# Optimization experiments

Hardware: AMD Instinct MI355X
Metric: run time of the kernel (lower is better)

The kernel has to match this reference:

```python
import jax, jax.numpy as jnp
import numpy as np

H = 16      # num_heads
D = 64      # head_dim
BQ = 64     # block_size_q
BKV = 64    # block_size_kv


def setup_inputs() -> dict:
    key = jax.random.key(0)
    ks = jax.random.split(key, 5)
    B, S, dim = 2, 2048, 1024
    x = jax.random.normal(ks[0], (B, S, dim), dtype=jnp.float32)
    Wq = jax.random.normal(ks[1], (dim, H * D), dtype=jnp.float32) * 0.02
    Wk = jax.random.normal(ks[2], (dim, H * D), dtype=jnp.float32) * 0.02
    Wv = jax.random.normal(ks[3], (dim, H * D), dtype=jnp.float32) * 0.02
    Wo = jax.random.normal(ks[4], (H * D, dim), dtype=jnp.float32) * 0.02
    return {"x": x, "Wq": Wq, "Wk": Wk, "Wv": Wv, "Wo": Wo}


def _flash_tiled(q, k, v, scale):
    # q,k,v: (B, H, S, D). Non-causal tiled attention with online softmax,
    # faithfully replicating the source's per-iteration division by l_new.
    B, nh, S, d = q.shape
    nq, nkv = S // BQ, S // BKV
    qb = q.reshape(B, nh, nq, BQ, d)                       # all q blocks at once (outer loop vectorized)
    kb = k.reshape(B, nh, nkv, BKV, d).transpose(2, 0, 1, 3, 4)  # (nkv, B, H, BKV, D)
    vb = v.reshape(B, nh, nkv, BKV, d).transpose(2, 0, 1, 3, 4)

    o0 = jnp.zeros((B, nh, nq, BQ, d), q.dtype)
    m0 = jnp.full((B, nh, nq, BQ), -jnp.inf, q.dtype)
    l0 = jnp.zeros((B, nh, nq, BQ), q.dtype)

    def step(carry, kv):
        o, m, l = carry
        kj, vj = kv
        s = jnp.einsum('bhnqd,bhkd->bhnqk', qb, kj) * scale   # (B,H,nq,BQ,BKV)
        m_new = jnp.maximum(m, s.max(axis=-1))
        p = jnp.exp(s - m_new[..., None])
        alpha = jnp.exp(m - m_new)
        l_new = alpha * l + p.sum(axis=-1)
        # NOTE: division by l_new every iteration, as in the source module.
        o_new = (alpha[..., None] * o + jnp.einsum('bhnqk,bhkd->bhnqd', p, vj)) / l_new[..., None]
        return (o_new, m_new, l_new), None

    (o, _, _), _ = jax.lax.scan(step, (o0, m0, l0), (kb, vb))
    return o.reshape(B, nh, S, d)


def reference(x, Wq, Wk, Wv, Wo):
    B, S, dim = x.shape
    scale = D ** -0.5
    q = (x @ Wq).reshape(B, S, H, D).transpose(0, 2, 1, 3)
    k = (x @ Wk).reshape(B, S, H, D).transpose(0, 2, 1, 3)
    v = (x @ Wv).reshape(B, S, H, D).transpose(0, 2, 1, 3)
    o = _flash_tiled(q, k, v, scale)                       # (B,H,S,D)
    out = o.transpose(0, 2, 1, 3).reshape(B, S, H * D)
    return out @ Wo
```

## Files before the change

### kernel.cpp

```cpp
#include <hip/hip_runtime.h>
#include <hip/hip_bf16.h>
#include <math.h>

#define BB   2
#define SS   2048
#define DIM  1024
#define NH   16
#define HD   64
#define MTOT (BB * SS)

typedef unsigned short ushortT;
typedef __attribute__((ext_vector_type(8))) short short8v;
typedef __attribute__((ext_vector_type(4))) float float4v;
typedef __attribute__((ext_vector_type(16))) float float16v;

union FragU { short8v v; unsigned short us[8]; unsigned int u[4]; };

__device__ inline unsigned short f2bf(float x) {
    unsigned u = __builtin_bit_cast(unsigned, x);
    u += 0x7fffu + ((u >> 16) & 1u);
    return (unsigned short)(u >> 16);
}
__device__ inline float bf2f(unsigned short h) {
    unsigned u = ((unsigned)h) << 16;
    return __builtin_bit_cast(float, u);
}
__device__ inline void split_tr(float x, unsigned short& hi, unsigned short& lo) {
    unsigned u = __builtin_bit_cast(unsigned, x);
    hi = (unsigned short)(u >> 16);
    float hf = __builtin_bit_cast(float, u & 0xffff0000u);
    lo = (unsigned short)(__builtin_bit_cast(unsigned, x - hf) >> 16);
}
__device__ inline void split4(const float4& x, short4& hi, short4& lo) {
    unsigned short h0 = f2bf(x.x), h1 = f2bf(x.y), h2 = f2bf(x.z), h3 = f2bf(x.w);
    hi = make_short4((short)h0, (short)h1, (short)h2, (short)h3);
    lo = make_short4((short)f2bf(x.x - bf2f(h0)), (short)f2bf(x.y - bf2f(h1)),
                     (short)f2bf(x.z - bf2f(h2)), (short)f2bf(x.w - bf2f(h3)));
}
__device__ inline void gld_lds16(const void* g, void* l) {
    __builtin_amdgcn_global_load_lds(
        (const __attribute__((address_space(1))) void*)g,
        (__attribute__((address_space(3))) void*)l, 16, 0, 0);
}
__device__ inline unsigned cvt_pk_bf16(float a, float b) {
    unsigned r;
    asm("v_cvt_pk_bf16_f32 %0, %1, %2" : "=v"(r) : "v"(a), "v"(b));
    return r;
}
__device__ inline void permlane32_swap(unsigned &a, unsigned &b) {
    asm("v_permlane32_swap_b32 %0, %1" : "+v"(a), "+v"(b));
}

__global__ __launch_bounds__(256) void convert_split_kernel(
    const float* __restrict__ in, ushortT* __restrict__ hi, ushortT* __restrict__ lo, int n4)
{
    int t = blockIdx.x * 256 + threadIdx.x;
    if (t < n4) {
        float4 x = ((const float4*)in)[t];
        short4 h, l; split4(x, h, l);
        ((short4*)hi)[t] = h;
        ((short4*)lo)[t] = l;
    }
}

__global__ __launch_bounds__(256) void transpose_split_kernel(
    const float* __restrict__ W0, const float* __restrict__ W1,
    const float* __restrict__ W2, const float* __restrict__ W3,
    ushortT* __restrict__ WtH, ushortT* __restrict__ WtL)
{
    const int z = blockIdx.z;
    const float* __restrict__ W = (z == 0) ? W0 : (z == 1) ? W1 : (z == 2) ? W2 : W3;
    ushortT* H = WtH + (size_t)z * 1024 * 1024;
    ushortT* L = WtL + (size_t)z * 1024 * 1024;

    __shared__ float T[64][65];
    const int k0 = blockIdx.y * 64, n0 = blockIdx.x * 64;
    const int tid = threadIdx.x;
    const int c4 = (tid & 15) * 4;

#pragma unroll
    for (int i = 0; i < 4; i++) {
        int r = (tid >> 4) + 16 * i;
        *(float4*)&T[r][c4] = *(const float4*)(W + (size_t)(k0 + r) * 1024 + n0 + c4);
    }
    __syncthreads();
#pragma unroll
    for (int i = 0; i < 4; i++) {
        int n = (tid >> 4) + 16 * i;
        float4 vv = make_float4(T[c4 + 0][n], T[c4 + 1][n], T[c4 + 2][n], T[c4 + 3][n]);
        short4 h, l; split4(vv, h, l);
        *(short4*)&H[(size_t)(n0 + n) * 1024 + k0 + c4] = h;
        *(short4*)&L[(size_t)(n0 + n) * 1024 + k0 + c4] = l;
    }
}

__global__ __launch_bounds__(256) void kv_convert_kernel(
    const float* __restrict__ kw,
    ushortT* __restrict__ KhG, ushortT* __restrict__ KlG)
{
    const int jb = blockIdx.x, bh = blockIdx.y;
    const int b = bh >> 4, h = bh & 15;

    __shared__ float T[64][68];
    const int tid = threadIdx.x;
    const size_t ibase = (size_t)b * SS * DIM + (size_t)h * HD + (size_t)(jb * 64) * DIM;
    const int c4 = (tid & 15) * 4;
#pragma unroll
    for (int i = 0; i < 4; i++) {
        int r = (tid >> 4) + 16 * i;
        *(float4*)&T[r][c4] = *(const float4*)(kw + ibase + (size_t)r * DIM + c4);
    }
    __syncthreads();

    ushortT* oh = KhG + (size_t)(bh * 32 + jb) * 4096;
    ushortT* ol = KlG + (size_t)(bh * 32 + jb) * 4096;

#pragma unroll
    for (int i = 0; i < 2; i++) {
        const int s = tid + i * 256;
        const int f = s >> 6;
        const int lane = s & 63;
        const int ds = f >> 1, kvt = f & 1;
        const int kv = kvt * 32 + (lane & 31);
        const int d0 = ds * 16 + (lane >> 5) * 8;
        ushortT hv[8], lv[8];
#pragma unroll
        for (int j = 0; j < 8; j++) split_tr(T[kv][d0 + j], hv[j], lv[j]);
        *(short4*)&oh[s * 8]     = *(short4*)&hv[0];
        *(short4*)&oh[s * 8 + 4] = *(short4*)&hv[4];
        *(short4*)&ol[s * 8]     = *(short4*)&lv[0];
        *(short4*)&ol[s * 8 + 4] = *(short4*)&lv[4];
    }
}

__global__ __launch_bounds__(256, 2) void gemm_bt_split_kernel(
    const ushortT* __restrict__ Ah, const ushortT* __restrict__ Al,
    const ushortT* __restrict__ BtH, const ushortT* __restrict__ BtL,
    float* __restrict__ Y0, float* __restrict__ Y1,
    ushortT* __restrict__ VhG, ushortT* __restrict__ VlG)
{
    const int z = blockIdx.z;
    const ushortT* __restrict__ Bh = BtH + (size_t)z * 1024 * 1024;
    const ushortT* __restrict__ Bl = BtL + (size_t)z * 1024 * 1024;

    const int K = 1024, N = 1024;
    const int m0 = blockIdx.y * 128;
    const int n0 = blockIdx.x * 128;

    __shared__ __align__(16) ushortT AhS[128 * 32];
    __shared__ __align__(16) ushortT AlS[128 * 32];
    __shared__ __align__(16) ushortT BhS[128 * 32];
    __shared__ __align__(16) ushortT BlS[128 * 32];

    const int tid  = threadIdx.x;
    const int wave = tid >> 6, lane = tid & 63;
    const int quad = lane >> 4, l15 = lane & 15;
    const int wm = wave >> 1, wn = wave & 1;

    const int s0 = tid, s1 = tid + 256;
    const int ar0 = s0 >> 2, ak0 = (s0 & 3) * 8;
    const int ar1 = s1 >> 2, ak1 = (s1 & 3) * 8;

    float4v acc[4][4];
#pragma unroll
    for (int i = 0; i < 4; i++)
#pragma unroll
        for (int j = 0; j < 4; j++) acc[i][j] = (float4v){0.f, 0.f, 0.f, 0.f};

    for (int k0 = 0; k0 < K; k0 += 32) {
        __syncthreads();
        gld_lds16(Ah + (size_t)(m0 + ar0) * K + k0 + ak0, &AhS[s0 * 8]);
        gld_lds16(Ah + (size_t)(m0 + ar1) * K + k0 + ak1, &AhS[s1 * 8]);
        gld_lds16(Al + (size_t)(m0 + ar0) * K + k0 + ak0, &AlS[s0 * 8]);
        gld_lds16(Al + (size_t)(m0 + ar1) * K + k0 + ak1, &AlS[s1 * 8]);
        gld_lds16(Bh + (size_t)(n0 + ar0) * K + k0 + ak0, &BhS[s0 * 8]);
        gld_lds16(Bh + (size_t)(n0 + ar1) * K + k0 + ak1, &BhS[s1 * 8]);
        gld_lds16(Bl + (size_t)(n0 + ar0) * K + k0 + ak0, &BlS[s0 * 8]);
        gld_lds16(Bl + (size_t)(n0 + ar1) * K + k0 + ak1, &BlS[s1 * 8]);
        __syncthreads();

        FragU ah[4], al[4], bh[4], bl[4];
#pragma unroll
        for (int t = 0; t < 4; t++) {
            ah[t].v = *(const short8v*)&AhS[(wm * 64 + t * 16 + l15) * 32 + quad * 8];
            al[t].v = *(const short8v*)&AlS[(wm * 64 + t * 16 + l15) * 32 + quad * 8];
            bh[t].v = *(const short8v*)&BhS[(wn * 64 + t * 16 + l15) * 32 + quad * 8];
            bl[t].v = *(const short8v*)&BlS[(wn * 64 + t * 16 + l15) * 32 + quad * 8];
        }
#pragma unroll
        for (int mt = 0; mt < 4; mt++)
#pragma unroll
            for (int nt = 0; nt < 4; nt++) {
                acc[mt][nt] = __builtin_amdgcn_mfma_f32_16x16x32_bf16(ah[mt].v, bh[nt].v, acc[mt][nt], 0, 0, 0);
                acc[mt][nt] = __builtin_amdgcn_mfma_f32_16x16x32_bf16(ah[mt].v, bl[nt].v, acc[mt][nt], 0, 0, 0);
                acc[mt][nt] = __builtin_amdgcn_mfma_f32_16x16x32_bf16(al[mt].v, bh[nt].v, acc[mt][nt], 0, 0, 0);
            }
    }

    if (z == 2) {
        const int b  = m0 >> 11;
        const int jb = ((m0 & 2047) >> 6) + wm;
        const int h  = (n0 >> 6) + wn;
        const size_t tb = (size_t)((b * 16 + h) * 32 + jb) * 4096;
        ushortT* vh = VhG + tb;
        ushortT* vl = VlG + tb;
#pragma unroll
        for (int mt = 0; mt < 4; mt++)
#pragma unroll
            for (int nt = 0; nt < 4; nt++) {
                const int off = ((((nt >> 1) * 4 + mt) * 64 +
                                  (quad >> 1) * 32 + (nt & 1) * 16 + l15) * 8) +
                                (quad & 1) * 4;
                float4 vv = make_float4(acc[mt][nt][0], acc[mt][nt][1],
                                        acc[mt][nt][2], acc[mt][nt][3]);
                unsigned short h0, l0, h1, l1, h2, l2, h3, l3;
                split_tr(vv.x, h0, l0); split_tr(vv.y, h1, l1);
                split_tr(vv.z, h2, l2); split_tr(vv.w, h3, l3);
                *(short4*)&vh[off] = make_short4((short)h0, (short)h1, (short)h2, (short)h3);
                *(short4*)&vl[off] = make_short4((short)l0, (short)l1, (short)l2, (short)l3);
            }
    } else {
        float* __restrict__ Y = (z == 0) ? Y0 : Y1;
#pragma unroll
        for (int mt = 0; mt < 4; mt++)
#pragma unroll
            for (int r = 0; r < 4; r++) {
                const int row = m0 + wm * 64 + mt * 16 + quad * 4 + r;
                float* yp = Y + (size_t)row * N + n0 + wn * 64 + l15;
#pragma unroll
                for (int nt = 0; nt < 4; nt++)
                    yp[nt * 16] = acc[mt][nt][r];
            }
    }
}

__global__ __launch_bounds__(256, 2) void attn_mfma_kernel(
    const float* __restrict__ q,
    const ushortT* __restrict__ KhG, const ushortT* __restrict__ KlG,
    const ushortT* __restrict__ VhG, const ushortT* __restrict__ VlG,
    ushortT* __restrict__ Oh, ushortT* __restrict__ Ol)
{
    __shared__ __align__(16) ushortT SMEM[32768];

    const int tid  = threadIdx.x;
    const int wave = tid >> 6, lane = tid & 63;
    const int l31 = lane & 31, hi5 = lane >> 5;
    const int bh = blockIdx.y, b = bh >> 4, h = bh & 15;
    const size_t base = (size_t)b * SS * DIM + (size_t)h * HD;
    const int qs0 = blockIdx.x * 128 + wave * 32;
    const int lane8 = lane * 8;
    const int sl0 = wave * 128 + lane, sl1 = sl0 + 64;

    ushortT* K0 = SMEM;
    ushortT* K1 = SMEM + 8192;
    ushortT* V0 = SMEM + 16384;
    ushortT* V1 = SMEM + 24576;

    const float qscale = 0.125f * 1.4426950408889634f;
    FragU Qh[4], Ql[4];
    {
        const int qrow = qs0 + l31;
#pragma unroll
        for (int ds = 0; ds < 4; ds++) {
            const float* p0 = q + base + (size_t)qrow * DIM + ds * 16 + hi5 * 8;
            float4 a = *(const float4*)(p0);
            float4 c = *(const float4*)(p0 + 4);
            float e[8] = {a.x, a.y, a.z, a.w, c.x, c.y, c.z, c.w};
#pragma unroll
            for (int j = 0; j < 8; j++) {
                float x = e[j] * qscale;
                unsigned short hs = f2bf(x);
                Qh[ds].us[j] = hs;
                Ql[ds].us[j] = f2bf(x - bf2f(hs));
            }
        }
    }

    float16v Oacc[2];
#pragma unroll
    for (int dt = 0; dt < 2; dt++)
        Oacc[dt] = (float16v){0.f,0.f,0.f,0.f,0.f,0.f,0.f,0.f,
                              0.f,0.f,0.f,0.f,0.f,0.f,0.f,0.f};

    float m_run = -INFINITY;
    float l_run = 0.f;

    auto stage_K = [&](int t, ushortT* dst) {
        const size_t tb = (size_t)(bh * 32 + t) * 4096;
        gld_lds16(KhG + tb + sl0 * 8, &dst[sl0 * 8]);
        gld_lds16(KhG + tb + sl1 * 8, &dst[sl1 * 8]);
        gld_lds16(KlG + tb + sl0 * 8, &dst[4096 + sl0 * 8]);
        gld_lds16(KlG + tb + sl1 * 8, &dst[4096 + sl1 * 8]);
    };
    auto stage_V = [&](int t, ushortT* dst) {
        const size_t tb = (size_t)(bh * 32 + t) * 4096;
        gld_lds16(VhG + tb + sl0 * 8, &dst[sl0 * 8]);
        gld_lds16(VhG + tb + sl1 * 8, &dst[sl1 * 8]);
        gld_lds16(VlG + tb + sl0 * 8, &dst[4096 + sl0 * 8]);
        gld_lds16(VlG + tb + sl1 * 8, &dst[4096 + sl1 * 8]);
    };

    auto qk = [&](const ushortT* Kb, float16v (&st)[2]) {
        const ushortT* KhS = Kb;
        const ushortT* KlS = Kb + 4096;
#pragma unroll
        for (int t = 0; t < 2; t++)
            st[t] = (float16v){0.f,0.f,0.f,0.f,0.f,0.f,0.f,0.f,
                               0.f,0.f,0.f,0.f,0.f,0.f,0.f,0.f};
#pragma unroll
        for (int ds = 0; ds < 4; ds++) {
            FragU kh0, kl0, kh1, kl1;
            kh0.v = *(const short8v*)&KhS[(ds * 2 + 0) * 512 + lane8];
            kl0.v = *(const short8v*)&KlS[(ds * 2 + 0) * 512 + lane8];
            kh1.v = *(const short8v*)&KhS[(ds * 2 + 1) * 512 + lane8];
            kl1.v = *(const short8v*)&KlS[(ds * 2 + 1) * 512 + lane8];
            st[0] = __builtin_amdgcn_mfma_f32_32x32x16_bf16(kh0.v, Qh[ds].v, st[0], 0, 0, 0);
            st[0] = __builtin_amdgcn_mfma_f32_32x32x16_bf16(kh0.v, Ql[ds].v, st[0], 0, 0, 0);
            st[0] = __builtin_amdgcn_mfma_f32_32x32x16_bf16(kl0.v, Qh[ds].v, st[0], 0, 0, 0);
            st[1] = __builtin_amdgcn_mfma_f32_32x32x16_bf16(kh1.v, Qh[ds].v, st[1], 0, 0, 0);
            st[1] = __builtin_amdgcn_mfma_f32_32x32x16_bf16(kh1.v, Ql[ds].v, st[1], 0, 0, 0);
            st[1] = __builtin_amdgcn_mfma_f32_32x32x16_bf16(kl1.v, Qh[ds].v, st[1], 0, 0, 0);
        }
    };

    auto finish = [&](float16v (&st)[2], const ushortT* Vb) {
        const ushortT* VhS = Vb;
        const ushortT* VlS = Vb + 4096;
        float oscale, inv;
        {
            float g[8];
#pragma unroll
            for (int t = 0; t < 2; t++)
#pragma unroll
                for (int i = 0; i < 4; i++)
                    g[t * 4 + i] = fmaxf(fmaxf(st[t][4 * i], st[t][4 * i + 1]),
                                         fmaxf(st[t][4 * i + 2], st[t][4 * i + 3]));
            float vmax = fmaxf(fmaxf(fmaxf(g[0], g[1]), fmaxf(g[2], g[3])),
                               fmaxf(fmaxf(g[4], g[5]), fmaxf(g[6], g[7])));
            vmax = fmaxf(vmax, __shfl_xor(vmax, 32, 64));
            const float mn = fmaxf(m_run, vmax);
            const float al = __builtin_amdgcn_exp2f(m_run - mn);

            float ssum = 0.f;
#pragma unroll
            for (int t = 0; t < 2; t++)
#pragma unroll
                for (int r = 0; r < 16; r++) {
                    const float p = __builtin_amdgcn_exp2f(st[t][r] - mn);
                    st[t][r] = p;
                    ssum += p;
                }
            ssum += __shfl_xor(ssum, 32, 64);
            const float ln = al * l_run + ssum;
            inv = __builtin_amdgcn_rcpf(ln);
            oscale = al * inv;
#pragma unroll
            for (int t = 0; t < 2; t++)
#pragma unroll
                for (int r = 0; r < 16; r++)
                    st[t][r] *= inv;
            m_run = mn;
            l_run = ln;
        }

#pragma unroll
        for (int dt = 0; dt < 2; dt++)
#pragma unroll
            for (int r = 0; r < 16; r++)
                Oacc[dt][r] *= oscale;

#pragma unroll
        for (int kvs = 0; kvs < 4; kvs++) {
            const int kvt = kvs >> 1;
            const int R = (kvs & 1) * 8;
            float p0 = st[kvt][R + 0], p1 = st[kvt][R + 1];
            float p2 = st[kvt][R + 2], p3 = st[kvt][R + 3];
            float p4 = st[kvt][R + 4], p5 = st[kvt][R + 5];
            float p6 = st[kvt][R + 6], p7 = st[kvt][R + 7];
            unsigned X0 = cvt_pk_bf16(p0, p1), X1 = cvt_pk_bf16(p2, p3);
            unsigned Y0 = cvt_pk_bf16(p4, p5), Y1 = cvt_pk_bf16(p6, p7);
            float e0 = p0 - __builtin_bit_cast(float, X0 << 16);
            float e1 = p1 - __builtin_bit_cast(float, X0 & 0xffff0000u);
            float e2 = p2 - __builtin_bit_cast(float, X1 << 16);
            float e3 = p3 - __builtin_bit_cast(float, X1 & 0xffff0000u);
            float e4 = p4 - __builtin_bit_cast(float, Y0 << 16);
            float e5 = p5 - __builtin_bit_cast(float, Y0 & 0xffff0000u);
            float e6 = p6 - __builtin_bit_cast(float, Y1 << 16);
            float e7 = p7 - __builtin_bit_cast(float, Y1 & 0xffff0000u);
            unsigned Z0 = cvt_pk_bf16(e0, e1), Z1 = cvt_pk_bf16(e2, e3);
            unsigned W0 = cvt_pk_bf16(e4, e5), W1 = cvt_pk_bf16(e6, e7);
            permlane32_swap(X0, Y0);
            permlane32_swap(X1, Y1);
            permlane32_swap(Z0, W0);
            permlane32_swap(Z1, W1);
            FragU Phf, Plf;
            Phf.u[0] = X0; Phf.u[1] = X1; Phf.u[2] = Y0; Phf.u[3] = Y1;
            Plf.u[0] = Z0; Plf.u[1] = Z1; Plf.u[2] = W0; Plf.u[3] = W1;

#pragma unroll
            for (int dt = 0; dt < 2; dt++) {
                FragU vh, vl;
                vh.v = *(const short8v*)&VhS[(dt * 4 + kvs) * 512 + lane8];
                vl.v = *(const short8v*)&VlS[(dt * 4 + kvs) * 512 + lane8];
                Oacc[dt] = __builtin_amdgcn_mfma_f32_32x32x16_bf16(vh.v, Phf.v, Oacc[dt], 0, 0, 0);
                Oacc[dt] = __builtin_amdgcn_mfma_f32_32x32x16_bf16(vl.v, Phf.v, Oacc[dt], 0, 0, 0);
                Oacc[dt] = __builtin_amdgcn_mfma_f32_32x32x16_bf16(vh.v, Plf.v, Oacc[dt], 0, 0, 0);
            }
        }
    };

    float16v stA[2], stB[2];

    stage_K(0, K0);
    stage_K(1, K1);
    stage_V(0, V0);
    __syncthreads();
    qk(K0, stA);
    __syncthreads();

    auto iter = [&](int jb, float16v (&SC)[2], float16v (&SN)[2],
                    ushortT* Kc, ushortT* Kn, ushortT* Vc, ushortT* Vn) {
        if (jb <= 29) stage_K(jb + 2, Kc);
        if (jb <= 30) stage_V(jb + 1, Vn);
        if (jb <= 30) qk(Kn, SN);
        finish(SC, Vc);
        __syncthreads();
    };

    for (int jb = 0; jb < 32; jb += 2) {
        iter(jb,     stA, stB, K0, K1, V0, V1);
        iter(jb + 1, stB, stA, K1, K0, V1, V0);
    }

    float* EP = ((float*)SMEM) + wave * 1056;
    const int qq = lane >> 1, dh = (lane & 1) * 16;
#pragma unroll
    for (int dt = 0; dt < 2; dt++) {
#pragma unroll
        for (int g = 0; g < 4; g++) {
            float4 wv = make_float4(Oacc[dt][4 * g + 0], Oacc[dt][4 * g + 1],
                                    Oacc[dt][4 * g + 2], Oacc[dt][4 * g + 3]);
            *(float4*)&EP[l31 * 33 + g * 8 + hi5 * 4] = wv;
        }
        float vals[16];
#pragma unroll
        for (int k4 = 0; k4 < 4; k4++)
            *(float4*)&vals[k4 * 4] = *(const float4*)&EP[qq * 33 + dh + k4 * 4];

        unsigned ho[8], lo8[8];
#pragma unroll
        for (int kk = 0; kk < 8; kk++) {
            unsigned short h0, l0, h1, l1;
            split_tr(vals[2 * kk], h0, l0);
            split_tr(vals[2 * kk + 1], h1, l1);
            ho[kk]  = (unsigned)h0 | ((unsigned)h1 << 16);
            lo8[kk] = (unsigned)l0 | ((unsigned)l1 << 16);
        }
        const int qrow = qs0 + qq;
        const size_t off = (size_t)(b * SS + qrow) * DIM + h * HD + dt * 32 + dh;
        *(uint4*)&Oh[off]     = make_uint4(ho[0], ho[1], ho[2], ho[3]);
        *(uint4*)&Oh[off + 8] = make_uint4(ho[4], ho[5], ho[6], ho[7]);
        *(uint4*)&Ol[off]     = make_uint4(lo8[0], lo8[1], lo8[2], lo8[3]);
        *(uint4*)&Ol[off + 8] = make_uint4(lo8[4], lo8[5], lo8[6], lo8[7]);
    }
}

extern "C" void kernel_launch(void* const* d_in, const int* in_sizes, int n_in,
                              void* d_out, int out_size, void* d_ws, size_t ws_size,
                              hipStream_t stream)
{
    const float* x  = (const float*)d_in[0];
    const float* Wq = (const float*)d_in[1];
    const float* Wk = (const float*)d_in[2];
    const float* Wv = (const float*)d_in[3];
    const float* Wo = (const float*)d_in[4];
    float* out = (float*)d_out;

    char* w = (char*)d_ws;
    float*   qw  = (float*)(w);
    float*   kw  = (float*)(w + ((size_t)16 << 20));
    ushortT* VhG = (ushortT*)(w + ((size_t)32 << 20));
    ushortT* VlG = (ushortT*)(w + ((size_t)40 << 20));
    ushortT* XhS = (ushortT*)(w + ((size_t)48 << 20));
    ushortT* XlS = (ushortT*)(w + ((size_t)56 << 20));
    ushortT* WtH = (ushortT*)(w + ((size_t)64 << 20));
    ushortT* WtL = (ushortT*)(w + ((size_t)72 << 20));
    ushortT* KhG = (ushortT*)(w + ((size_t)80 << 20));
    ushortT* KlG = (ushortT*)(w + ((size_t)88 << 20));
    ushortT* OhS = (ushortT*)kw;
    ushortT* OlS = (ushortT*)(w + ((size_t)24 << 20));

    dim3 blk(256);
    const int n4 = MTOT * DIM / 4;

    convert_split_kernel<<<dim3(n4 / 256), blk, 0, stream>>>(x, XhS, XlS, n4);
    transpose_split_kernel<<<dim3(16, 16, 4), blk, 0, stream>>>(Wq, Wk, Wv, Wo, WtH, WtL);

    gemm_bt_split_kernel<<<dim3(8, 32, 3), blk, 0, stream>>>(
        XhS, XlS, WtH, WtL, qw, kw, VhG, VlG);

    kv_convert_kernel<<<dim3(32, 32), blk, 0, stream>>>(kw, KhG, KlG);

    attn_mfma_kernel<<<dim3(16, 32), blk, 0, stream>>>(qw, KhG, KlG, VhG, VlG, OhS, OlS);

    gemm_bt_split_kernel<<<dim3(8, 32, 1), blk, 0, stream>>>(
        OhS, OlS, WtH + (size_t)3 * 1024 * 1024, WtL + (size_t)3 * 1024 * 1024,
        out, nullptr, nullptr, nullptr);
}
```

Baseline: 319.4 us.

## Fuse K split/layout conversion into QKV GEMM epilogue and prioritize MFMA waves

The separate kv_convert kernel is removed. The QKV GEMM's K-projection epilogue now stages each wave's tile through a new shared-memory buffer and writes the bf16 hi/lo split directly in the attention fragment layout. This avoids a kernel launch and a full fp32 K round-trip through global memory. It also wraps the attention MFMA groups in s_setprio and hoists the V fragment loads ahead of the MFMAs. The extra 34KB of LDS in the GEMM kernel may reduce its occupancy below the two blocks per CU targeted by its launch bounds.

```diff
diff --git a/kernel.cpp b/kernel.cpp
--- a/kernel.cpp
+++ b/kernel.cpp
@@ -94,50 +94,12 @@
     }
 }
 
-__global__ __launch_bounds__(256) void kv_convert_kernel(
-    const float* __restrict__ kw,
-    ushortT* __restrict__ KhG, ushortT* __restrict__ KlG)
-{
-    const int jb = blockIdx.x, bh = blockIdx.y;
-    const int b = bh >> 4, h = bh & 15;
-
-    __shared__ float T[64][68];
-    const int tid = threadIdx.x;
-    const size_t ibase = (size_t)b * SS * DIM + (size_t)h * HD + (size_t)(jb * 64) * DIM;
-    const int c4 = (tid & 15) * 4;
-#pragma unroll
-    for (int i = 0; i < 4; i++) {
-        int r = (tid >> 4) + 16 * i;
-        *(float4*)&T[r][c4] = *(const float4*)(kw + ibase + (size_t)r * DIM + c4);
-    }
-    __syncthreads();
-
-    ushortT* oh = KhG + (size_t)(bh * 32 + jb) * 4096;
-    ushortT* ol = KlG + (size_t)(bh * 32 + jb) * 4096;
-
-#pragma unroll
-    for (int i = 0; i < 2; i++) {
-        const int s = tid + i * 256;
-        const int f = s >> 6;
-        const int lane = s & 63;
-        const int ds = f >> 1, kvt = f & 1;
-        const int kv = kvt * 32 + (lane & 31);
-        const int d0 = ds * 16 + (lane >> 5) * 8;
-        ushortT hv[8], lv[8];
-#pragma unroll
-        for (int j = 0; j < 8; j++) split_tr(T[kv][d0 + j], hv[j], lv[j]);
-        *(short4*)&oh[s * 8]     = *(short4*)&hv[0];
-        *(short4*)&oh[s * 8 + 4] = *(short4*)&hv[4];
-        *(short4*)&ol[s * 8]     = *(short4*)&lv[0];
-        *(short4*)&ol[s * 8 + 4] = *(short4*)&lv[4];
-    }
-}
-
 __global__ __launch_bounds__(256, 2) void gemm_bt_split_kernel(
     const ushortT* __restrict__ Ah, const ushortT* __restrict__ Al,
     const ushortT* __restrict__ BtH, const ushortT* __restrict__ BtL,
     float* __restrict__ Y0, float* __restrict__ Y1,
-    ushortT* __restrict__ VhG, ushortT* __restrict__ VlG)
+    ushortT* __restrict__ VhG, ushortT* __restrict__ VlG,
+    ushortT* __restrict__ KhGp, ushortT* __restrict__ KlGp)
 {
     const int z = blockIdx.z;
     const ushortT* __restrict__ Bh = BtH + (size_t)z * 1024 * 1024;
@@ -151,10 +113,12 @@
     __shared__ __align__(16) ushortT AlS[128 * 32];
     __shared__ __align__(16) ushortT BhS[128 * 32];
     __shared__ __align__(16) ushortT BlS[128 * 32];
+    __shared__ __align__(16) float EPI[4][32][68];
 
     const int tid  = threadIdx.x;
     const int wave = tid >> 6, lane = tid & 63;
     const int quad = lane >> 4, l15 = lane & 15;
+    const int l31 = lane & 31, hi5g = lane >> 5;
     const int wm = wave >> 1, wn = wave & 1;
 
     const int s0 = tid, s1 = tid + 256;
@@ -219,6 +183,39 @@
                 *(short4*)&vh[off] = make_short4((short)h0, (short)h1, (short)h2, (short)h3);
                 *(short4*)&vl[off] = make_short4((short)l0, (short)l1, (short)l2, (short)l3);
             }
+    } else if (z == 1 && KhGp != nullptr) {
+        const int b  = m0 >> 11;
+        const int jb = ((m0 & 2047) >> 6) + wm;
+        const int h  = (n0 >> 6) + wn;
+        const size_t tb = (size_t)((b * 16 + h) * 32 + jb) * 4096;
+        float (*EP)[68] = EPI[wave];
+#pragma unroll
+        for (int kvt = 0; kvt < 2; kvt++) {
+#pragma unroll
+            for (int mh = 0; mh < 2; mh++) {
+                const int mt = kvt * 2 + mh;
+#pragma unroll
+                for (int nt = 0; nt < 4; nt++)
+#pragma unroll
+                    for (int r = 0; r < 4; r++)
+                        EP[mh * 16 + quad * 4 + r][nt * 16 + l15] = acc[mt][nt][r];
+            }
+#pragma unroll
+            for (int ds = 0; ds < 4; ds++) {
+                const int d0 = ds * 16 + hi5g * 8;
+                float4 va = *(const float4*)&EP[l31][d0];
+                float4 vb = *(const float4*)&EP[l31][d0 + 4];
+                float ev[8] = {va.x, va.y, va.z, va.w, vb.x, vb.y, vb.z, vb.w};
+                ushortT hv[8], lv[8];
+#pragma unroll
+                for (int j = 0; j < 8; j++) split_tr(ev[j], hv[j], lv[j]);
+                const size_t o8 = tb + (size_t)(ds * 2 + kvt) * 512 + lane * 8;
+                *(short4*)&KhGp[o8]     = *(short4*)&hv[0];
+                *(short4*)&KhGp[o8 + 4] = *(short4*)&hv[4];
+                *(short4*)&KlGp[o8]     = *(short4*)&lv[0];
+                *(short4*)&KlGp[o8 + 4] = *(short4*)&lv[4];
+            }
+        }
     } else {
         float* __restrict__ Y = (z == 0) ? Y0 : Y1;
 #pragma unroll
@@ -314,12 +311,14 @@
             kl0.v = *(const short8v*)&KlS[(ds * 2 + 0) * 512 + lane8];
             kh1.v = *(const short8v*)&KhS[(ds * 2 + 1) * 512 + lane8];
             kl1.v = *(const short8v*)&KlS[(ds * 2 + 1) * 512 + lane8];
+            __builtin_amdgcn_s_setprio(1);
             st[0] = __builtin_amdgcn_mfma_f32_32x32x16_bf16(kh0.v, Qh[ds].v, st[0], 0, 0, 0);
             st[0] = __builtin_amdgcn_mfma_f32_32x32x16_bf16(kh0.v, Ql[ds].v, st[0], 0, 0, 0);
             st[0] = __builtin_amdgcn_mfma_f32_32x32x16_bf16(kl0.v, Qh[ds].v, st[0], 0, 0, 0);
             st[1] = __builtin_amdgcn_mfma_f32_32x32x16_bf16(kh1.v, Qh[ds].v, st[1], 0, 0, 0);
             st[1] = __builtin_amdgcn_mfma_f32_32x32x16_bf16(kh1.v, Ql[ds].v, st[1], 0, 0, 0);
             st[1] = __builtin_amdgcn_mfma_f32_32x32x16_bf16(kl1.v, Qh[ds].v, st[1], 0, 0, 0);
+            __builtin_amdgcn_s_setprio(0);
         }
     };
 
@@ -397,15 +396,19 @@
             Phf.u[0] = X0; Phf.u[1] = X1; Phf.u[2] = Y0; Phf.u[3] = Y1;
             Plf.u[0] = Z0; Plf.u[1] = Z1; Plf.u[2] = W0; Plf.u[3] = W1;
 
-#pragma unroll
-            for (int dt = 0; dt < 2; dt++) {
-                FragU vh, vl;
-                vh.v = *(const short8v*)&VhS[(dt * 4 + kvs) * 512 + lane8];
-                vl.v = *(const short8v*)&VlS[(dt * 4 + kvs) * 512 + lane8];
-                Oacc[dt] = __builtin_amdgcn_mfma_f32_32x32x16_bf16(vh.v, Phf.v, Oacc[dt], 0, 0, 0);
-                Oacc[dt] = __builtin_amdgcn_mfma_f32_32x32x16_bf16(vl.v, Phf.v, Oacc[dt], 0, 0, 0);
-                Oacc[dt] = __builtin_amdgcn_mfma_f32_32x32x16_bf16(vh.v, Plf.v, Oacc[dt], 0, 0, 0);
-            }
+            FragU vh0, vl0, vh1, vl1;
+            vh0.v = *(const short8v*)&VhS[(0 * 4 + kvs) * 512 + lane8];
+            vl0.v = *(const short8v*)&VlS[(0 * 4 + kvs) * 512 + lane8];
+            vh1.v = *(const short8v*)&VhS[(1 * 4 + kvs) * 512 + lane8];
+            vl1.v = *(const short8v*)&VlS[(1 * 4 + kvs) * 512 + lane8];
+            __builtin_amdgcn_s_setprio(1);
+            Oacc[0] = __builtin_amdgcn_mfma_f32_32x32x16_bf16(vh0.v, Phf.v, Oacc[0], 0, 0, 0);
+            Oacc[0] = __builtin_amdgcn_mfma_f32_32x32x16_bf16(vl0.v, Phf.v, Oacc[0], 0, 0, 0);
+            Oacc[0] = __builtin_amdgcn_mfma_f32_32x32x16_bf16(vh0.v, Plf.v, Oacc[0], 0, 0, 0);
+            Oacc[1] = __builtin_amdgcn_mfma_f32_32x32x16_bf16(vh1.v, Phf.v, Oacc[1], 0, 0, 0);
+            Oacc[1] = __builtin_amdgcn_mfma_f32_32x32x16_bf16(vl1.v, Phf.v, Oacc[1], 0, 0, 0);
+            Oacc[1] = __builtin_amdgcn_mfma_f32_32x32x16_bf16(vh1.v, Plf.v, Oacc[1], 0, 0, 0);
+            __builtin_amdgcn_s_setprio(0);
         }
     };
 
@@ -497,13 +500,11 @@
     transpose_split_kernel<<<dim3(16, 16, 4), blk, 0, stream>>>(Wq, Wk, Wv, Wo, WtH, WtL);
 
     gemm_bt_split_kernel<<<dim3(8, 32, 3), blk, 0, stream>>>(
-        XhS, XlS, WtH, WtL, qw, kw, VhG, VlG);
-
-    kv_convert_kernel<<<dim3(32, 32), blk, 0, stream>>>(kw, KhG, KlG);
+        XhS, XlS, WtH, WtL, qw, nullptr, VhG, VlG, KhG, KlG);
 
     attn_mfma_kernel<<<dim3(16, 32), blk, 0, stream>>>(qw, KhG, KlG, VhG, VlG, OhS, OlS);
 
     gemm_bt_split_kernel<<<dim3(8, 32, 1), blk, 0, stream>>>(
         OhS, OlS, WtH + (size_t)3 * 1024 * 1024, WtL + (size_t)3 * 1024 * 1024,
-        out, nullptr, nullptr, nullptr);
-}
+        out, nullptr, nullptr, nullptr, nullptr, nullptr);
+}
```

Measured after the change: 336.5 us. 1.05x slower.
